# Optimization experiments

Hardware: AMD Instinct MI355X
Metric: run time of the kernel (lower is better)

## Reference

```python
import jax, jax.numpy as jnp
import numpy as np


def setup_inputs() -> dict:
    key = jax.random.key(0)
    k1, k2 = jax.random.split(key)
    N, C, T, K = 8192, 3, 2048, 10
    Xt = jax.random.normal(k1, (N, C, T), dtype=jnp.float32)
    y_true = jax.random.randint(k2, (N,), 0, K, dtype=jnp.int64)
    return {"Xt": Xt, "y_true": y_true, "num_classes": K}


def reference(Xt, y_true, num_classes):
    # Within-Class Sum of Squares: for each class k,
    #   loss_k = mean((Xk - mean(Xk, axis=0))**2)  (mean over all elements)
    # total = mean over classes. Assumes all num_classes labels are present
    # (matches torch.unique iteration under this data distribution).
    N = Xt.shape[0]
    D = Xt.shape[1] * Xt.shape[2]  # elements per sample
    sums = jax.ops.segment_sum(Xt, y_true, num_segments=num_classes)        # [K, C, T]
    counts = jax.ops.segment_sum(jnp.ones((N,), Xt.dtype), y_true,
                                 num_segments=num_classes)                  # [K]
    means = sums / counts[:, None, None]                                    # [K, C, T]
    sq = jnp.square(Xt - means[y_true])                                     # [N, C, T]
    sq_per_sample = sq.reshape(N, -1).sum(axis=1)                           # [N]
    sq_sums = jax.ops.segment_sum(sq_per_sample, y_true,
                                  num_segments=num_classes)                 # [K]
    per_class_mse = sq_sums / (counts * D)                                  # [K]
    return per_class_mse.mean()
```

## Files before the change

kernel.cpp:

```cpp
#include <hip/hip_runtime.h>

#define N_SAMP 8192
#define D_DIM 6144
#define K_CLS 10
#define CHUNK 32
#define NCHUNKS (N_SAMP / CHUNK)
#define COLS_PER_BLOCK 1024
#define NGROUPS (D_DIM / COLS_PER_BLOCK)
#define PIPE 8

__global__ __launch_bounds__(256) void build_sort(const int* __restrict__ y,
                                                  int* __restrict__ counts,
                                                  int* __restrict__ sorted,
                                                  float* __restrict__ S1,
                                                  float* __restrict__ s2sum,
                                                  float* __restrict__ out) {
    __shared__ int M[K_CLS * 256];
    __shared__ int wsum[4];
    const int tid = threadIdx.x;
    const int lane = tid & 63;
    const int wid = tid >> 6;

    for (int j = tid; j < K_CLS * D_DIM; j += 256) S1[j] = 0.0f;
    if (tid < K_CLS) s2sum[tid] = 0.0f;
    if (tid == 0) out[0] = 0.0f;

    int h[K_CLS];
#pragma unroll
    for (int k = 0; k < K_CLS; ++k) h[k] = 0;
    const int base = tid * 32;
#pragma unroll 1
    for (int i = 0; i < 32; ++i) {
        const int yy = y[base + i];
#pragma unroll
        for (int k = 0; k < K_CLS; ++k) h[k] += (yy == k) ? 1 : 0;
    }
#pragma unroll
    for (int k = 0; k < K_CLS; ++k) M[k * 256 + tid] = h[k];
    __syncthreads();

    int loc[10];
    int run = 0;
#pragma unroll
    for (int j = 0; j < 10; ++j) { loc[j] = run; run += M[tid * 10 + j]; }
    int v = run;
#pragma unroll
    for (int d = 1; d < 64; d <<= 1) {
        int n = __shfl_up(v, d, 64);
        if (lane >= d) v += n;
    }
    if (lane == 63) wsum[wid] = v;
    __syncthreads();
    int wbase = 0;
#pragma unroll
    for (int w = 0; w < 4; ++w) wbase += (w < wid) ? wsum[w] : 0;
    const int tbase = wbase + (v - run);
    __syncthreads();
#pragma unroll
    for (int j = 0; j < 10; ++j) M[tid * 10 + j] = tbase + loc[j];
    __syncthreads();

    if (tid < K_CLS) {
        const int s = M[tid * 256];
        const int e = (tid == K_CLS - 1) ? N_SAMP : M[(tid + 1) * 256];
        counts[tid] = e - s;
    }

    int off[K_CLS];
#pragma unroll
    for (int k = 0; k < K_CLS; ++k) off[k] = M[k * 256 + tid];
#pragma unroll 1
    for (int i = 0; i < 32; ++i) {
        const int yy = y[base + i];
#pragma unroll
        for (int k = 0; k < K_CLS; ++k)
            if (yy == k) sorted[off[k]++] = (k << 16) | (base + i);
    }
}

__global__ __launch_bounds__(256) void wcss_accum(const float* __restrict__ X,
                                                  const int* __restrict__ sorted,
                                                  float* __restrict__ S1,
                                                  float* __restrict__ s2sum) {
    __shared__ int idx_lds[CHUNK];
    __shared__ int cls_lds[CHUNK];
    const int tid = threadIdx.x;
    const int col0 = blockIdx.x * COLS_PER_BLOCK + tid * 4;
    const int s0g = blockIdx.y * CHUNK;

    if (tid < CHUNK) {
        const int p = sorted[s0g + tid];
        idx_lds[tid] = p & 0xffff;
        cls_lds[tid] = p >> 16;
    }
    __syncthreads();

    const float* base = X + col0;
    float4 a1 = make_float4(0.f, 0.f, 0.f, 0.f);
    float s2c = 0.f;
    int kcur = __builtin_amdgcn_readfirstlane(cls_lds[0]);

    float4 buf[PIPE];
#pragma unroll
    for (int j = 0; j < PIPE; ++j)
        buf[j] = *(const float4*)(base + (size_t)idx_lds[j] * D_DIM);

#pragma unroll
    for (int s = 0; s < CHUNK; ++s) {
        const float4 v = buf[s & (PIPE - 1)];
        if (s + PIPE < CHUNK)
            buf[s & (PIPE - 1)] =
                *(const float4*)(base + (size_t)idx_lds[s + PIPE] * D_DIM);

        const int yk = __builtin_amdgcn_readfirstlane(cls_lds[s]);
        if (yk != kcur) {
            float* b1 = S1 + kcur * D_DIM + col0;
            atomicAdd(b1 + 0, a1.x); atomicAdd(b1 + 1, a1.y);
            atomicAdd(b1 + 2, a1.z); atomicAdd(b1 + 3, a1.w);
            atomicAdd(&s2sum[kcur], s2c);
            a1 = make_float4(0.f, 0.f, 0.f, 0.f);
            s2c = 0.f;
            kcur = yk;
        }
        a1.x += v.x; a1.y += v.y; a1.z += v.z; a1.w += v.w;
        s2c += v.x * v.x + v.y * v.y + v.z * v.z + v.w * v.w;
    }

    float* b1 = S1 + kcur * D_DIM + col0;
    atomicAdd(b1 + 0, a1.x); atomicAdd(b1 + 1, a1.y);
    atomicAdd(b1 + 2, a1.z); atomicAdd(b1 + 3, a1.w);
    atomicAdd(&s2sum[kcur], s2c);
}

__global__ __launch_bounds__(256) void wcss_finish(const float* __restrict__ S1,
                                                   const float* __restrict__ s2sum,
                                                   const int* __restrict__ counts,
                                                   float* __restrict__ out) {
    __shared__ float sbuf[256];
    const int tid = threadIdx.x;
    const int k = blockIdx.x / NGROUPS;
    const int g = blockIdx.x % NGROUPS;
    const float cnt = (float)counts[k];
    const float inv = 1.0f / (cnt * cnt * (float)D_DIM * (float)K_CLS);

    const float4 v = *(const float4*)(S1 + k * D_DIM + g * COLS_PER_BLOCK + tid * 4);
    float t = -(v.x * v.x + v.y * v.y + v.z * v.z + v.w * v.w) * inv;
    if (g == 0 && tid == 0)
        t += s2sum[k] / (cnt * (float)D_DIM * (float)K_CLS);

    sbuf[tid] = t;
    __syncthreads();
    for (int off = 128; off > 0; off >>= 1) {
        if (tid < off) sbuf[tid] += sbuf[tid + off];
        __syncthreads();
    }
    if (tid == 0) atomicAdd(out, sbuf[0]);
}

extern "C" void kernel_launch(void* const* d_in, const int* in_sizes, int n_in,
                              void* d_out, int out_size, void* d_ws, size_t ws_size,
                              hipStream_t stream) {
    const float* X = (const float*)d_in[0];
    const int* y = (const int*)d_in[1];

    float* S1 = (float*)d_ws;
    float* s2sum = S1 + K_CLS * D_DIM;
    int* counts = (int*)(s2sum + K_CLS);
    int* sorted = counts + K_CLS;
    float* out = (float*)d_out;

    build_sort<<<dim3(1), dim3(256), 0, stream>>>(y, counts, sorted, S1, s2sum, out);
    wcss_accum<<<dim3(NGROUPS, NCHUNKS), dim3(256), 0, stream>>>(X, sorted, S1, s2sum);
    wcss_finish<<<dim3(K_CLS * NGROUPS), dim3(256), 0, stream>>>(S1, s2sum, counts, out);
}
```

Baseline: 352.4 us.

## Split work into per-class runs and parallelize sort across 1024 threads

The sort kernel now uses 1024 threads, reads labels with vector loads and zeroes S1 with float4 stores. It also emits a table of class-aligned runs of up to 64 samples, so each accumulation block handles exactly one class and never has to check for a class change. Within each block, the per-block s2 sum is reduced by a wave and block reduction before one atomic, which cuts atomic traffic. The cost is one serial thread building the run table, plus padding blocks that exit early. It also relies on the number of runs fitting in the fixed limit of 144.

Result: faster. 299.9 us (-14.9%).

```diff
diff --git a/kernel.cpp b/kernel.cpp
--- a/kernel.cpp
+++ b/kernel.cpp
@@ -3,46 +3,50 @@
 #define N_SAMP 8192
 #define D_DIM 6144
 #define K_CLS 10
-#define CHUNK 32
-#define NCHUNKS (N_SAMP / CHUNK)
+#define CHUNK 64
 #define COLS_PER_BLOCK 1024
 #define NGROUPS (D_DIM / COLS_PER_BLOCK)
+#define MAXRUNS 144
 #define PIPE 8
 
-__global__ __launch_bounds__(256) void build_sort(const int* __restrict__ y,
-                                                  int* __restrict__ counts,
-                                                  int* __restrict__ sorted,
-                                                  float* __restrict__ S1,
-                                                  float* __restrict__ s2sum,
-                                                  float* __restrict__ out) {
-    __shared__ int M[K_CLS * 256];
-    __shared__ int wsum[4];
+__global__ __launch_bounds__(1024) void build_sort(const int* __restrict__ y,
+                                                   int* __restrict__ counts,
+                                                   int* __restrict__ sorted,
+                                                   int2* __restrict__ runs,
+                                                   float* __restrict__ S1,
+                                                   float* __restrict__ s2sum,
+                                                   float* __restrict__ out) {
+    __shared__ int M[K_CLS * 1024];
+    __shared__ int wsum[16];
+    __shared__ int Bnd[K_CLS + 1];
     const int tid = threadIdx.x;
     const int lane = tid & 63;
     const int wid = tid >> 6;
 
-    for (int j = tid; j < K_CLS * D_DIM; j += 256) S1[j] = 0.0f;
-    if (tid < K_CLS) s2sum[tid] = 0.0f;
-    if (tid == 0) out[0] = 0.0f;
-
+    const float4 z4 = make_float4(0.f, 0.f, 0.f, 0.f);
+    for (int j = tid; j < K_CLS * D_DIM / 4; j += 1024) ((float4*)S1)[j] = z4;
+    if (tid < K_CLS) s2sum[tid] = 0.f;
+    if (tid == 0) out[0] = 0.f;
+
+    const int base = tid * 8;
+    const int4 ya = ((const int4*)y)[tid * 2];
+    const int4 yb = ((const int4*)y)[tid * 2 + 1];
+    int yy[8] = {ya.x, ya.y, ya.z, ya.w, yb.x, yb.y, yb.z, yb.w};
     int h[K_CLS];
 #pragma unroll
     for (int k = 0; k < K_CLS; ++k) h[k] = 0;
-    const int base = tid * 32;
-#pragma unroll 1
-    for (int i = 0; i < 32; ++i) {
-        const int yy = y[base + i];
-#pragma unroll
-        for (int k = 0; k < K_CLS; ++k) h[k] += (yy == k) ? 1 : 0;
-    }
-#pragma unroll
-    for (int k = 0; k < K_CLS; ++k) M[k * 256 + tid] = h[k];
-    __syncthreads();
-
-    int loc[10];
+#pragma unroll
+    for (int i = 0; i < 8; ++i)
+#pragma unroll
+        for (int k = 0; k < K_CLS; ++k) h[k] += (yy[i] == k) ? 1 : 0;
+#pragma unroll
+    for (int k = 0; k < K_CLS; ++k) M[k * 1024 + tid] = h[k];
+    __syncthreads();
+
+    int loc[K_CLS];
     int run = 0;
 #pragma unroll
-    for (int j = 0; j < 10; ++j) { loc[j] = run; run += M[tid * 10 + j]; }
+    for (int j = 0; j < K_CLS; ++j) { loc[j] = run; run += M[tid * K_CLS + j]; }
     int v = run;
 #pragma unroll
     for (int d = 1; d < 64; d <<= 1) {
@@ -53,83 +57,104 @@
     __syncthreads();
     int wbase = 0;
 #pragma unroll
-    for (int w = 0; w < 4; ++w) wbase += (w < wid) ? wsum[w] : 0;
+    for (int w = 0; w < 16; ++w) wbase += (w < wid) ? wsum[w] : 0;
     const int tbase = wbase + (v - run);
     __syncthreads();
 #pragma unroll
-    for (int j = 0; j < 10; ++j) M[tid * 10 + j] = tbase + loc[j];
-    __syncthreads();
-
-    if (tid < K_CLS) {
-        const int s = M[tid * 256];
-        const int e = (tid == K_CLS - 1) ? N_SAMP : M[(tid + 1) * 256];
-        counts[tid] = e - s;
+    for (int j = 0; j < K_CLS; ++j) M[tid * K_CLS + j] = tbase + loc[j];
+    __syncthreads();
+
+    if (tid < K_CLS) Bnd[tid] = M[tid * 1024];
+    if (tid == 0) Bnd[K_CLS] = N_SAMP;
+    __syncthreads();
+    if (tid < K_CLS) counts[tid] = Bnd[tid + 1] - Bnd[tid];
+
+    if (tid == 0) {
+        int r = 0;
+        for (int k = 0; k < K_CLS; ++k)
+            for (int p = Bnd[k]; p < Bnd[k + 1]; p += CHUNK) {
+                int l = Bnd[k + 1] - p;
+                if (l > CHUNK) l = CHUNK;
+                runs[r++] = make_int2(p, l);
+            }
+        for (; r < MAXRUNS; ++r) runs[r] = make_int2(0, 0);
     }
 
     int off[K_CLS];
 #pragma unroll
-    for (int k = 0; k < K_CLS; ++k) off[k] = M[k * 256 + tid];
-#pragma unroll 1
-    for (int i = 0; i < 32; ++i) {
-        const int yy = y[base + i];
+    for (int k = 0; k < K_CLS; ++k) off[k] = M[k * 1024 + tid];
+#pragma unroll
+    for (int i = 0; i < 8; ++i)
 #pragma unroll
         for (int k = 0; k < K_CLS; ++k)
-            if (yy == k) sorted[off[k]++] = (k << 16) | (base + i);
-    }
+            if (yy[i] == k) sorted[off[k]++] = (k << 16) | (base + i);
 }
 
 __global__ __launch_bounds__(256) void wcss_accum(const float* __restrict__ X,
                                                   const int* __restrict__ sorted,
+                                                  const int2* __restrict__ runs,
                                                   float* __restrict__ S1,
                                                   float* __restrict__ s2sum) {
-    __shared__ int idx_lds[CHUNK];
-    __shared__ int cls_lds[CHUNK];
+    __shared__ int off_lds[CHUNK];
+    __shared__ int cls0;
+    __shared__ float wred[4];
     const int tid = threadIdx.x;
-    const int col0 = blockIdx.x * COLS_PER_BLOCK + tid * 4;
-    const int s0g = blockIdx.y * CHUNK;
-
-    if (tid < CHUNK) {
-        const int p = sorted[s0g + tid];
-        idx_lds[tid] = p & 0xffff;
-        cls_lds[tid] = p >> 16;
-    }
-    __syncthreads();
-
-    const float* base = X + col0;
+    const int lane = tid & 63;
+    const int wid = tid >> 6;
+
+    const int2 rn = runs[blockIdx.y];
+    const int len = rn.y;
+    if (len == 0) return;
+
+    if (tid < CHUNK && tid < len) {
+        const int p = sorted[rn.x + tid];
+        off_lds[tid] = (p & 0xffff) * (D_DIM * (int)sizeof(float));
+        if (tid == 0) cls0 = p >> 16;
+    }
+    __syncthreads();
+    const int kcls = __builtin_amdgcn_readfirstlane(cls0);
+    const char* basep = (const char*)(X + blockIdx.x * COLS_PER_BLOCK + tid * 4);
+
     float4 a1 = make_float4(0.f, 0.f, 0.f, 0.f);
     float s2c = 0.f;
-    int kcur = __builtin_amdgcn_readfirstlane(cls_lds[0]);
 
     float4 buf[PIPE];
 #pragma unroll
+    for (int j = 0; j < PIPE; ++j) {
+        const int ix = (j < len) ? j : len - 1;
+        buf[j] = *(const float4*)(basep + (size_t)off_lds[ix]);
+    }
+
+    int s8 = 0;
+#pragma unroll 1
+    for (; s8 + PIPE <= len; s8 += PIPE) {
+#pragma unroll
+        for (int j = 0; j < PIPE; ++j) {
+            const float4 v = buf[j];
+            int nx = s8 + PIPE + j;
+            nx = (nx < len) ? nx : len - 1;
+            buf[j] = *(const float4*)(basep + (size_t)off_lds[nx]);
+            a1.x += v.x; a1.y += v.y; a1.z += v.z; a1.w += v.w;
+            s2c += v.x * v.x + v.y * v.y + v.z * v.z + v.w * v.w;
+        }
+    }
+#pragma unroll
     for (int j = 0; j < PIPE; ++j)
-        buf[j] = *(const float4*)(base + (size_t)idx_lds[j] * D_DIM);
-
-#pragma unroll
-    for (int s = 0; s < CHUNK; ++s) {
-        const float4 v = buf[s & (PIPE - 1)];
-        if (s + PIPE < CHUNK)
-            buf[s & (PIPE - 1)] =
-                *(const float4*)(base + (size_t)idx_lds[s + PIPE] * D_DIM);
-
-        const int yk = __builtin_amdgcn_readfirstlane(cls_lds[s]);
-        if (yk != kcur) {
-            float* b1 = S1 + kcur * D_DIM + col0;
-            atomicAdd(b1 + 0, a1.x); atomicAdd(b1 + 1, a1.y);
-            atomicAdd(b1 + 2, a1.z); atomicAdd(b1 + 3, a1.w);
-            atomicAdd(&s2sum[kcur], s2c);
-            a1 = make_float4(0.f, 0.f, 0.f, 0.f);
-            s2c = 0.f;
-            kcur = yk;
+        if (s8 + j < len) {
+            const float4 v = buf[j];
+            a1.x += v.x; a1.y += v.y; a1.z += v.z; a1.w += v.w;
+            s2c += v.x * v.x + v.y * v.y + v.z * v.z + v.w * v.w;
         }
-        a1.x += v.x; a1.y += v.y; a1.z += v.z; a1.w += v.w;
-        s2c += v.x * v.x + v.y * v.y + v.z * v.z + v.w * v.w;
-    }
-
-    float* b1 = S1 + kcur * D_DIM + col0;
+
+    float* b1 = S1 + kcls * D_DIM + blockIdx.x * COLS_PER_BLOCK + tid * 4;
     atomicAdd(b1 + 0, a1.x); atomicAdd(b1 + 1, a1.y);
     atomicAdd(b1 + 2, a1.z); atomicAdd(b1 + 3, a1.w);
-    atomicAdd(&s2sum[kcur], s2c);
+
+#pragma unroll
+    for (int o = 32; o > 0; o >>= 1) s2c += __shfl_down(s2c, o, 64);
+    if (lane == 0) wred[wid] = s2c;
+    __syncthreads();
+    if (tid == 0) atomicAdd(&s2sum[kcls], wred[0] + wred[1] + wred[2] + wred[3]);
 }
 
 __global__ __launch_bounds__(256) void wcss_finish(const float* __restrict__ S1,
@@ -167,9 +192,13 @@
     float* s2sum = S1 + K_CLS * D_DIM;
     int* counts = (int*)(s2sum + K_CLS);
     int* sorted = counts + K_CLS;
+    int2* runs = (int2*)(sorted + N_SAMP);
     float* out = (float*)d_out;
 
-    build_sort<<<dim3(1), dim3(256), 0, stream>>>(y, counts, sorted, S1, s2sum, out);
-    wcss_accum<<<dim3(NGROUPS, NCHUNKS), dim3(256), 0, stream>>>(X, sorted, S1, s2sum);
-    wcss_finish<<<dim3(K_CLS * NGROUPS), dim3(256), 0, stream>>>(S1, s2sum, counts, out);
-}
+    build_sort<<<dim3(1), dim3(1024), 0, stream>>>(y, counts, sorted, runs,
+                                                   S1, s2sum, out);
+    wcss_accum<<<dim3(NGROUPS, MAXRUNS), dim3(256), 0, stream>>>(X, sorted, runs,
+                                                                 S1, s2sum);
+    wcss_finish<<<dim3(K_CLS * NGROUPS), dim3(256), 0, stream>>>(S1, s2sum,
+                                                                 counts, out);
+}
```

## Parallelize label sort, memset accumulators, and block-reduce sum-of-squares atomics

Applied to the files above, without the earlier changes.

The single-block sort now runs with 1024 threads, each handling 8 labels loaded as vector int4s, so its serial scalar loops shrink. Zeroing of the accumulators moves out of that block into hipMemsetAsync calls. In the accumulation kernel the per-thread atomicAdd on the per-class sum of squares is replaced by a wave-shuffle plus LDS block reduction, cutting contention on the 10 scalar addresses. Row offsets are also precomputed in bytes. The tradeoff is extra __syncthreads at each class boundary and two added memset launches.

Result: faster. 297.3 us (-15.6%).

```diff
diff --git a/kernel.cpp b/kernel.cpp
--- a/kernel.cpp
+++ b/kernel.cpp
@@ -4,45 +4,39 @@
 #define D_DIM 6144
 #define K_CLS 10
 #define CHUNK 32
-#define NCHUNKS (N_SAMP / CHUNK)
+#define NWIN (N_SAMP / CHUNK)
 #define COLS_PER_BLOCK 1024
 #define NGROUPS (D_DIM / COLS_PER_BLOCK)
 #define PIPE 8
 
-__global__ __launch_bounds__(256) void build_sort(const int* __restrict__ y,
-                                                  int* __restrict__ counts,
-                                                  int* __restrict__ sorted,
-                                                  float* __restrict__ S1,
-                                                  float* __restrict__ s2sum,
-                                                  float* __restrict__ out) {
-    __shared__ int M[K_CLS * 256];
-    __shared__ int wsum[4];
+__global__ __launch_bounds__(1024) void build_sort(const int* __restrict__ y,
+                                                   int* __restrict__ counts,
+                                                   int* __restrict__ sorted) {
+    __shared__ int M[K_CLS * 1024];
+    __shared__ int wsum[16];
     const int tid = threadIdx.x;
     const int lane = tid & 63;
     const int wid = tid >> 6;
 
-    for (int j = tid; j < K_CLS * D_DIM; j += 256) S1[j] = 0.0f;
-    if (tid < K_CLS) s2sum[tid] = 0.0f;
-    if (tid == 0) out[0] = 0.0f;
-
+    const int base = tid * 8;
+    const int4 ya = ((const int4*)y)[tid * 2];
+    const int4 yb = ((const int4*)y)[tid * 2 + 1];
+    int yy[8] = {ya.x, ya.y, ya.z, ya.w, yb.x, yb.y, yb.z, yb.w};
     int h[K_CLS];
 #pragma unroll
     for (int k = 0; k < K_CLS; ++k) h[k] = 0;
-    const int base = tid * 32;
-#pragma unroll 1
-    for (int i = 0; i < 32; ++i) {
-        const int yy = y[base + i];
 #pragma unroll
-        for (int k = 0; k < K_CLS; ++k) h[k] += (yy == k) ? 1 : 0;
-    }
+    for (int i = 0; i < 8; ++i)
 #pragma unroll
-    for (int k = 0; k < K_CLS; ++k) M[k * 256 + tid] = h[k];
+        for (int k = 0; k < K_CLS; ++k) h[k] += (yy[i] == k) ? 1 : 0;
+#pragma unroll
+    for (int k = 0; k < K_CLS; ++k) M[k * 1024 + tid] = h[k];
     __syncthreads();
 
-    int loc[10];
+    int loc[K_CLS];
     int run = 0;
 #pragma unroll
-    for (int j = 0; j < 10; ++j) { loc[j] = run; run += M[tid * 10 + j]; }
+    for (int j = 0; j < K_CLS; ++j) { loc[j] = run; run += M[tid * K_CLS + j]; }
     int v = run;
 #pragma unroll
     for (int d = 1; d < 64; d <<= 1) {
@@ -53,49 +47,49 @@
     __syncthreads();
     int wbase = 0;
 #pragma unroll
-    for (int w = 0; w < 4; ++w) wbase += (w < wid) ? wsum[w] : 0;
+    for (int w = 0; w < 16; ++w) wbase += (w < wid) ? wsum[w] : 0;
     const int tbase = wbase + (v - run);
     __syncthreads();
 #pragma unroll
-    for (int j = 0; j < 10; ++j) M[tid * 10 + j] = tbase + loc[j];
+    for (int j = 0; j < K_CLS; ++j) M[tid * K_CLS + j] = tbase + loc[j];
     __syncthreads();
 
     if (tid < K_CLS) {
-        const int s = M[tid * 256];
-        const int e = (tid == K_CLS - 1) ? N_SAMP : M[(tid + 1) * 256];
+        const int s = M[tid * 1024];
+        const int e = (tid == K_CLS - 1) ? N_SAMP : M[(tid + 1) * 1024];
         counts[tid] = e - s;
     }
 
     int off[K_CLS];
 #pragma unroll
-    for (int k = 0; k < K_CLS; ++k) off[k] = M[k * 256 + tid];
-#pragma unroll 1
-    for (int i = 0; i < 32; ++i) {
-        const int yy = y[base + i];
+    for (int k = 0; k < K_CLS; ++k) off[k] = M[k * 1024 + tid];
+#pragma unroll
+    for (int i = 0; i < 8; ++i)
 #pragma unroll
         for (int k = 0; k < K_CLS; ++k)
-            if (yy == k) sorted[off[k]++] = (k << 16) | (base + i);
-    }
+            if (yy[i] == k) sorted[off[k]++] = (k << 16) | (base + i);
 }
 
 __global__ __launch_bounds__(256) void wcss_accum(const float* __restrict__ X,
                                                   const int* __restrict__ sorted,
                                                   float* __restrict__ S1,
                                                   float* __restrict__ s2sum) {
-    __shared__ int idx_lds[CHUNK];
+    __shared__ int off_lds[CHUNK];
     __shared__ int cls_lds[CHUNK];
+    __shared__ float wred[4];
     const int tid = threadIdx.x;
+    const int lane = tid & 63;
+    const int wid = tid >> 6;
     const int col0 = blockIdx.x * COLS_PER_BLOCK + tid * 4;
-    const int s0g = blockIdx.y * CHUNK;
 
     if (tid < CHUNK) {
-        const int p = sorted[s0g + tid];
-        idx_lds[tid] = p & 0xffff;
+        const int p = sorted[blockIdx.y * CHUNK + tid];
+        off_lds[tid] = (p & 0xffff) * (D_DIM * (int)sizeof(float));
         cls_lds[tid] = p >> 16;
     }
     __syncthreads();
 
-    const float* base = X + col0;
+    const char* basep = (const char*)(X + col0);
     float4 a1 = make_float4(0.f, 0.f, 0.f, 0.f);
     float s2c = 0.f;
     int kcur = __builtin_amdgcn_readfirstlane(cls_lds[0]);
@@ -103,21 +97,28 @@
     float4 buf[PIPE];
 #pragma unroll
     for (int j = 0; j < PIPE; ++j)
-        buf[j] = *(const float4*)(base + (size_t)idx_lds[j] * D_DIM);
+        buf[j] = *(const float4*)(basep + (size_t)off_lds[j]);
 
 #pragma unroll
     for (int s = 0; s < CHUNK; ++s) {
         const float4 v = buf[s & (PIPE - 1)];
         if (s + PIPE < CHUNK)
             buf[s & (PIPE - 1)] =
-                *(const float4*)(base + (size_t)idx_lds[s + PIPE] * D_DIM);
+                *(const float4*)(basep + (size_t)off_lds[s + PIPE]);
 
         const int yk = __builtin_amdgcn_readfirstlane(cls_lds[s]);
         if (yk != kcur) {
             float* b1 = S1 + kcur * D_DIM + col0;
             atomicAdd(b1 + 0, a1.x); atomicAdd(b1 + 1, a1.y);
             atomicAdd(b1 + 2, a1.z); atomicAdd(b1 + 3, a1.w);
-            atomicAdd(&s2sum[kcur], s2c);
+            float r = s2c;
+#pragma unroll
+            for (int o = 32; o > 0; o >>= 1) r += __shfl_down(r, o, 64);
+            if (lane == 0) wred[wid] = r;
+            __syncthreads();
+            if (tid == 0)
+                atomicAdd(&s2sum[kcur], wred[0] + wred[1] + wred[2] + wred[3]);
+            __syncthreads();
             a1 = make_float4(0.f, 0.f, 0.f, 0.f);
             s2c = 0.f;
             kcur = yk;
@@ -129,7 +130,12 @@
     float* b1 = S1 + kcur * D_DIM + col0;
     atomicAdd(b1 + 0, a1.x); atomicAdd(b1 + 1, a1.y);
     atomicAdd(b1 + 2, a1.z); atomicAdd(b1 + 3, a1.w);
-    atomicAdd(&s2sum[kcur], s2c);
+#pragma unroll
+    for (int o = 32; o > 0; o >>= 1) s2c += __shfl_down(s2c, o, 64);
+    if (lane == 0) wred[wid] = s2c;
+    __syncthreads();
+    if (tid == 0)
+        atomicAdd(&s2sum[kcur], wred[0] + wred[1] + wred[2] + wred[3]);
 }
 
 __global__ __launch_bounds__(256) void wcss_finish(const float* __restrict__ S1,
@@ -169,7 +175,11 @@
     int* sorted = counts + K_CLS;
     float* out = (float*)d_out;
 
-    build_sort<<<dim3(1), dim3(256), 0, stream>>>(y, counts, sorted, S1, s2sum, out);
-    wcss_accum<<<dim3(NGROUPS, NCHUNKS), dim3(256), 0, stream>>>(X, sorted, S1, s2sum);
-    wcss_finish<<<dim3(K_CLS * NGROUPS), dim3(256), 0, stream>>>(S1, s2sum, counts, out);
+    hipMemsetAsync(S1, 0, (K_CLS * D_DIM + K_CLS) * sizeof(float), stream);
+    hipMemsetAsync(out, 0, sizeof(float), stream);
+
+    build_sort<<<dim3(1), dim3(1024), 0, stream>>>(y, counts, sorted);
+    wcss_accum<<<dim3(NGROUPS, NWIN), dim3(256), 0, stream>>>(X, sorted, S1, s2sum);
+    wcss_finish<<<dim3(K_CLS * NGROUPS), dim3(256), 0, stream>>>(S1, s2sum,
+                                                                 counts, out);
 }
```
